# Performance work log

Measured on AMD Instinct MI355X. Metric: run time of the kernel, lower is better.

The kernel has to match this reference:

```python
import jax, jax.numpy as jnp
import numpy as np

D_MODEL = 1024
D_FF = 2 * D_MODEL
N_EXPERTS = 8
TOP_K = 2
SCAT_SCALE = 0.1


def setup_inputs() -> dict:
    key = jax.random.key(0)
    ks = jax.random.split(key, 8)
    s_in = 1.0 / np.sqrt(D_MODEL)
    s_ff = 1.0 / np.sqrt(D_FF)
    return {
        "x": jax.random.normal(ks[0], (4, 2048, D_MODEL), dtype=jnp.float32),
        "Wg": jax.random.uniform(ks[1], (D_MODEL, N_EXPERTS), minval=-s_in, maxval=s_in),
        "bg": jax.random.uniform(ks[2], (N_EXPERTS,), minval=-s_in, maxval=s_in),
        "W1": jax.random.uniform(ks[3], (N_EXPERTS, D_MODEL, D_FF), minval=-s_in, maxval=s_in),
        "b1": jax.random.uniform(ks[4], (N_EXPERTS, D_FF), minval=-s_in, maxval=s_in),
        "W2": jax.random.uniform(ks[5], (N_EXPERTS, D_FF, D_MODEL), minval=-s_ff, maxval=s_ff),
        "b2": jax.random.uniform(ks[6], (N_EXPERTS, D_MODEL), minval=-s_ff, maxval=s_ff),
    }


def reference(x, Wg, bg, W1, b1, W2, b2):
    B, N, D = x.shape
    T = B * N
    xf = x.reshape(T, D)

    # gating logits + norm-based modulation (scattering_scale branch)
    logits = xf @ Wg + bg  # [T, E]
    tnorm = jnp.linalg.norm(xf, axis=-1, keepdims=True)  # [T, 1]
    norm_scaled = (tnorm - tnorm.mean()) / (jnp.std(tnorm, ddof=1) + 1e-6)
    logits = logits + SCAT_SCALE * norm_scaled

    # top-k routing
    topv, topi = jax.lax.top_k(logits, TOP_K)  # [T, K]
    gates_k = jax.nn.softmax(topv, axis=-1)  # [T, K]
    routing_entropy = -(gates_k * jnp.log(jnp.clip(gates_k, 1e-8, None))).sum(-1).mean()

    # dense per-token expert-weight matrix (zeros for non-selected experts)
    E = W1.shape[0]
    gates = jnp.zeros((T, E), dtype=gates_k.dtype).at[
        jnp.arange(T)[:, None], topi
    ].add(gates_k)  # [T, E]

    # all-expert MLP (dense equivalent of sparse dispatch; weight 0 -> no contribution)
    h = jax.nn.relu(jnp.einsum("td,edf->etf", xf, W1) + b1[:, None, :])  # [E, T, F]
    y = jnp.einsum("etf,efd->etd", h, W2) + b2[:, None, :]  # [E, T, D]
    out = jnp.einsum("etd,te->td", y, gates).reshape(B, N, D)
    return out, routing_entropy
```

## Files before the change

### kernel.cpp

```cpp
#include <hip/hip_runtime.h>
#include <hip/hip_bf16.h>

#define T_TOK 8192
#define DMODEL 1024
#define DFF 2048
#define NEXP 8

typedef __attribute__((ext_vector_type(8))) short short8v;
typedef __attribute__((ext_vector_type(4))) float floatx4;
typedef __attribute__((ext_vector_type(4))) ushort ushort4v;

__device__ __forceinline__ ushort f2bf(float f) {
  union { float f; unsigned u; } v; v.f = f;
  unsigned u = v.u;
  unsigned r = (u + 0x7FFFu + ((u >> 16) & 1u)) >> 16;
  return (ushort)r;
}
__device__ __forceinline__ float bf2f(ushort b) {
  union { unsigned u; float f; } v; v.u = ((unsigned)b) << 16;
  return v.f;
}
__device__ __forceinline__ void gload16(const void* g, void* l) {
  __builtin_amdgcn_global_load_lds(
      (const __attribute__((address_space(1))) unsigned int*)g,
      (__attribute__((address_space(3))) unsigned int*)l, 16, 0, 0);
}
__device__ __forceinline__ short8v dsr128(unsigned off) {
  short8v r;
  asm volatile("ds_read_b128 %0, %1" : "=v"(r) : "v"(off));
  return r;
}
#define VMW(n) asm volatile("s_waitcnt vmcnt(" #n ")" ::: "memory")
#define LG0()  asm volatile("s_waitcnt lgkmcnt(0)" ::: "memory")
#define BAR()  asm volatile("s_barrier" ::: "memory")
#define SB0()  __builtin_amdgcn_sched_barrier(0)

__global__ void init_kernel(int* __restrict__ meta, float* __restrict__ entWs) {
  if (threadIdx.x < 64) meta[threadIdx.x] = 0;
  if (threadIdx.x == 0) *entWs = 0.f;
}

__global__ __launch_bounds__(256) void gating_kernel(
    const float* __restrict__ x, const float* __restrict__ Wg,
    const float* __restrict__ bg, int* __restrict__ meta,
    int* __restrict__ te, float* __restrict__ tg, float* __restrict__ entWs,
    ushort* __restrict__ xb) {
  __shared__ float wgT[8448];
  __shared__ float sbg[NEXP];
  __shared__ int cnt_s[NEXP];
  __shared__ float ent_s;
  int tid = threadIdx.x;
#pragma unroll
  for (int k = 0; k < 8; ++k) {
    int g4 = tid + 256 * k;
    float4 v = ((const float4*)Wg)[g4];
    int q = g4 * 4;
    int f = q >> 5;
    wgT[q + f]     = v.x;
    wgT[q + 1 + f] = v.y;
    wgT[q + 2 + f] = v.z;
    wgT[q + 3 + f] = v.w;
  }
  if (tid < NEXP) { sbg[tid] = bg[tid]; cnt_s[tid] = 0; }
  if (tid == 0) ent_s = 0.f;
  __syncthreads();

  int wid = tid >> 6, lane = tid & 63;
#pragma unroll 1
  for (int it = 0; it < 4; ++it) {
    int t = blockIdx.x * 16 + wid * 4 + it;
    const float* xr = x + (long)t * DMODEL;
    ushort* xbr = xb + (long)t * DMODEL;
    float acc[NEXP];
#pragma unroll
    for (int e = 0; e < NEXP; ++e) acc[e] = 0.f;
#pragma unroll
    for (int i = 0; i < 4; ++i) {
      int dbase = i * 256 + lane * 4;
      int pad = i * 64 + lane;
      float4 xv = *(const float4*)(xr + dbase);
      ushort4v s;
      s[0] = f2bf(xv.x); s[1] = f2bf(xv.y); s[2] = f2bf(xv.z); s[3] = f2bf(xv.w);
      *(ushort4v*)(xbr + dbase) = s;
      float xj[4] = {xv.x, xv.y, xv.z, xv.w};
#pragma unroll
      for (int j = 0; j < 4; ++j) {
        int base = 8 * (dbase + j) + pad;
#pragma unroll
        for (int e = 0; e < NEXP; ++e) acc[e] += xj[j] * wgT[base + e];
      }
    }
#pragma unroll
    for (int off = 32; off; off >>= 1)
#pragma unroll
      for (int e = 0; e < NEXP; ++e) acc[e] += __shfl_xor(acc[e], off, 64);
    if (lane == 0) {
      float lg[NEXP];
#pragma unroll
      for (int e = 0; e < NEXP; ++e) lg[e] = acc[e] + sbg[e];
      int e1 = 0; float v1 = lg[0];
#pragma unroll
      for (int e = 1; e < NEXP; ++e) if (lg[e] > v1) { v1 = lg[e]; e1 = e; }
      int e2 = -1; float v2 = -1e30f;
#pragma unroll
      for (int e = 0; e < NEXP; ++e) if (e != e1 && lg[e] > v2) { v2 = lg[e]; e2 = e; }
      float p2 = expf(v2 - v1);
      float s = 1.f + p2;
      float g1 = 1.f / s, g2 = p2 / s;
      float ent = -(g1 * logf(fmaxf(g1, 1e-8f)) + g2 * logf(fmaxf(g2, 1e-8f)));
      atomicAdd(&cnt_s[e1], 1);
      atomicAdd(&cnt_s[e2], 1);
      atomicAdd(&ent_s, ent);
      te[2 * t] = e1; te[2 * t + 1] = e2;
      tg[2 * t] = g1; tg[2 * t + 1] = g2;
    }
  }
  __syncthreads();
  if (tid < NEXP && cnt_s[tid]) atomicAdd(&meta[tid], cnt_s[tid]);
  if (tid == 0) atomicAdd(entWs, ent_s * (1.f / T_TOK));
}

__global__ void prefix_kernel(int* __restrict__ meta) {
  if (threadIdx.x == 0) {
    int s = 0;
    for (int e = 0; e < NEXP; ++e) { meta[16 + e] = s; s += meta[e]; meta[32 + e] = 0; }
  }
}

__global__ void scatter_kernel(const int* __restrict__ te, const float* __restrict__ tg,
                               int* __restrict__ meta, int* __restrict__ tok,
                               float* __restrict__ gate, int* __restrict__ slotOf) {
  int t = blockIdx.x * blockDim.x + threadIdx.x;
  if (t >= T_TOK) return;
  for (int k = 0; k < 2; ++k) {
    int e = te[2 * t + k];
    int pos = atomicAdd(&meta[32 + e], 1);
    int slot = meta[16 + e] + pos;
    tok[slot] = t;
    gate[slot] = tg[2 * t + k];
    slotOf[2 * t + k] = slot;
  }
}

__global__ __launch_bounds__(256) void tcvt_kernel(const float* __restrict__ src,
                                                   ushort* __restrict__ dst,
                                                   int R, int C) {
  __shared__ ushort tile[64][72];
  int tid = threadIdx.x;
  long eoff = (long)blockIdx.z * R * C;
  int r0 = blockIdx.y * 64, c0 = blockIdx.x * 64;
  int lr = tid >> 4, lc = (tid & 15) * 4;
#pragma unroll
  for (int p = 0; p < 4; ++p) {
    int r = lr + p * 16;
    float4 v = *(const float4*)&src[eoff + (long)(r0 + r) * C + (c0 + lc)];
    tile[r][lc + 0] = f2bf(v.x); tile[r][lc + 1] = f2bf(v.y);
    tile[r][lc + 2] = f2bf(v.z); tile[r][lc + 3] = f2bf(v.w);
  }
  __syncthreads();
  int sr = tid >> 3, sc = (tid & 7) * 8;
#pragma unroll
  for (int p = 0; p < 2; ++p) {
    int c = sr + p * 32;
    short8v v;
#pragma unroll
    for (int j = 0; j < 8; ++j) v[j] = (short)tile[sc + j][c];
    *(short8v*)&dst[eoff + (long)(c0 + c) * R + (r0 + sc)] = v;
  }
}

__device__ __forceinline__ void gemm_pipe(
    int NT, const char* aP0, const char* aP1,
    const char* bP0, const char* bP1, const char* bP2, const char* bP3,
    char* lds, int tid, floatx4 (&acc)[8][4]) {
  const unsigned ldsU = (unsigned)(unsigned long)lds;
  int lane = tid & 63, wid = tid >> 6;
  int lr = lane & 15, lg = lane >> 4;
  unsigned offA[8], offB[4];
#pragma unroll
  for (int mi = 0; mi < 8; ++mi) {
    int row = mi * 16 + lr;
    offA[mi] = row * 64 + ((lg * 16) ^ (((row >> 1) & 3) << 4));
  }
#pragma unroll
  for (int ni = 0; ni < 4; ++ni) {
    int row = wid * 64 + ni * 16 + lr;
    offB[ni] = row * 64 + ((lg * 16) ^ (((row >> 1) & 3) << 4));
  }

  auto STG_A = [&](int b, int t) {
    int koff = t * 64;
    char* d = lds + b * 8192;
    gload16(aP0 + koff, d + tid * 16);
    gload16(aP1 + koff, d + 4096 + tid * 16);
  };
  auto STG_B = [&](int b, int t) {
    int koff = t * 64;
    char* d = lds + 24576 + b * 16384;
    gload16(bP0 + koff, d + tid * 16);
    gload16(bP1 + koff, d + 4096 + tid * 16);
    gload16(bP2 + koff, d + 8192 + tid * 16);
    gload16(bP3 + koff, d + 12288 + tid * 16);
  };
  auto RDA = [&](int b, int mi) {
    return dsr128(ldsU + (unsigned)(b * 8192) + offA[mi]);
  };
  auto RDB = [&](int b, int ni) {
    return dsr128(ldsU + (unsigned)(24576 + b * 16384) + offB[ni]);
  };
  auto MM = [&](int mh, short8v* af, short8v* bf) {
#pragma unroll
    for (int mi = 0; mi < 4; ++mi)
#pragma unroll
      for (int ni = 0; ni < 4; ++ni)
        acc[mh * 4 + mi][ni] =
            __builtin_amdgcn_mfma_f32_16x16x32_bf16(af[mi], bf[ni], acc[mh * 4 + mi][ni], 0, 0, 0);
  };

  STG_A(0, 0); STG_B(0, 0);
  STG_A(1, 1); STG_B(1, 1);
  VMW(6); BAR();

  short8v af[4], bf[4];
  int b = 0;
  for (int t = 0; t + 2 < NT; ++t) {
    int bs = (b == 0) ? 2 : b - 1;
#pragma unroll
    for (int ni = 0; ni < 4; ++ni) bf[ni] = RDB(b, ni);
#pragma unroll
    for (int i = 0; i < 4; ++i) af[i] = RDA(b, i);
    STG_A(bs, t + 2);
    BAR(); LG0(); SB0();
    __builtin_amdgcn_s_setprio(1); MM(0, af, bf); __builtin_amdgcn_s_setprio(0);
    SB0(); BAR();
#pragma unroll
    for (int i = 0; i < 4; ++i) af[i] = RDA(b, 4 + i);
    STG_B(bs, t + 2);
    VMW(6);
    BAR(); LG0(); SB0();
    __builtin_amdgcn_s_setprio(1); MM(1, af, bf); __builtin_amdgcn_s_setprio(0);
    SB0(); BAR();
    b = (b == 2) ? 0 : b + 1;
  }
  {
#pragma unroll
    for (int ni = 0; ni < 4; ++ni) bf[ni] = RDB(b, ni);
#pragma unroll
    for (int i = 0; i < 4; ++i) af[i] = RDA(b, i);
    BAR(); LG0(); SB0();
    __builtin_amdgcn_s_setprio(1); MM(0, af, bf); __builtin_amdgcn_s_setprio(0);
    SB0(); BAR();
#pragma unroll
    for (int i = 0; i < 4; ++i) af[i] = RDA(b, 4 + i);
    VMW(0);
    BAR(); LG0(); SB0();
    __builtin_amdgcn_s_setprio(1); MM(1, af, bf); __builtin_amdgcn_s_setprio(0);
    SB0(); BAR();
    b = (b == 2) ? 0 : b + 1;
  }
  {
#pragma unroll
    for (int ni = 0; ni < 4; ++ni) bf[ni] = RDB(b, ni);
#pragma unroll
    for (int i = 0; i < 4; ++i) af[i] = RDA(b, i);
    BAR(); LG0(); SB0();
    __builtin_amdgcn_s_setprio(1); MM(0, af, bf); __builtin_amdgcn_s_setprio(0);
    SB0(); BAR();
#pragma unroll
    for (int i = 0; i < 4; ++i) af[i] = RDA(b, 4 + i);
    LG0(); SB0();
    __builtin_amdgcn_s_setprio(1); MM(1, af, bf); __builtin_amdgcn_s_setprio(0);
  }
}

__global__ __launch_bounds__(256, 2) void gemm1_kernel(
    const ushort* __restrict__ xb, const ushort* __restrict__ w1t,
    const float* __restrict__ b1, const int* __restrict__ meta,
    const int* __restrict__ tok, ushort* __restrict__ h) {
  const int NWG = 64 * 8 * NEXP;
  int flat = blockIdx.x;
  int wgid = (flat % 8) * (NWG / 8) + flat / 8;
  int m0 = (wgid & 63) * 128;
  int rest = wgid >> 6;
  int n0 = (rest & 7) * 256;
  int e = rest >> 3;
  int cnt = meta[e];
  if (m0 >= cnt) return;
  int bas = meta[16 + e];
  __shared__ char lds[73728];
  int tid = threadIdx.x;

  const char* w1e = (const char*)(w1t + (long)e * DFF * DMODEL);
  int rA = tid >> 2;
  int ch = tid & 3;
  auto sc = [&](int row) { return (unsigned)((ch * 16) ^ (((row >> 1) & 3) << 4)); };
  int ma0 = m0 + rA;        if (ma0 >= cnt) ma0 = cnt - 1;
  int ma1 = m0 + rA + 64;   if (ma1 >= cnt) ma1 = cnt - 1;
  const char* aP0 = (const char*)xb + (long)tok[bas + ma0] * (DMODEL * 2) + sc(rA);
  const char* aP1 = (const char*)xb + (long)tok[bas + ma1] * (DMODEL * 2) + sc(rA + 64);
  const char* bP0 = w1e + (long)(n0 + rA) * (DMODEL * 2) + sc(rA);
  const char* bP1 = w1e + (long)(n0 + rA + 64) * (DMODEL * 2) + sc(rA + 64);
  const char* bP2 = w1e + (long)(n0 + rA + 128) * (DMODEL * 2) + sc(rA + 128);
  const char* bP3 = w1e + (long)(n0 + rA + 192) * (DMODEL * 2) + sc(rA + 192);

  floatx4 acc[8][4];
#pragma unroll
  for (int i = 0; i < 8; ++i)
#pragma unroll
    for (int j = 0; j < 4; ++j) acc[i][j] = (floatx4){0.f, 0.f, 0.f, 0.f};

  gemm_pipe(DMODEL / 32, aP0, aP1, bP0, bP1, bP2, bP3, lds, tid, acc);

  int lane = tid & 63, wid = tid >> 6;
  int lr = lane & 15, lg = lane >> 4;
  const float* b1e = b1 + e * DFF;
#pragma unroll
  for (int mi = 0; mi < 8; ++mi) {
#pragma unroll
    for (int r = 0; r < 4; ++r) {
      int m = m0 + mi * 16 + lg * 4 + r;
      if (m >= cnt) continue;
      long hrow = (long)(bas + m) * DFF;
#pragma unroll
      for (int ni = 0; ni < 4; ++ni) {
        int f = n0 + wid * 64 + ni * 16 + lr;
        float v = acc[mi][ni][r] + b1e[f];
        h[hrow + f] = f2bf(fmaxf(v, 0.f));
      }
    }
  }
}

__global__ __launch_bounds__(256, 2) void gemm2_kernel(
    const ushort* __restrict__ h, const ushort* __restrict__ w2t,
    const float* __restrict__ b2, const int* __restrict__ meta,
    const float* __restrict__ gate, ushort* __restrict__ y) {
  const int NWG = 64 * 4 * NEXP;
  int flat = blockIdx.x;
  int wgid = (flat % 8) * (NWG / 8) + flat / 8;
  int m0 = (wgid & 63) * 128;
  int rest = wgid >> 6;
  int n0 = (rest & 3) * 256;
  int e = rest >> 2;
  int cnt = meta[e];
  if (m0 >= cnt) return;
  int bas = meta[16 + e];
  __shared__ char lds[73728];
  int tid = threadIdx.x;

  const char* w2e = (const char*)(w2t + (long)e * DMODEL * DFF);
  int rA = tid >> 2;
  int ch = tid & 3;
  auto sc = [&](int row) { return (unsigned)((ch * 16) ^ (((row >> 1) & 3) << 4)); };
  int ma0 = m0 + rA;        if (ma0 >= cnt) ma0 = cnt - 1;
  int ma1 = m0 + rA + 64;   if (ma1 >= cnt) ma1 = cnt - 1;
  const char* aP0 = (const char*)h + (long)(bas + ma0) * (DFF * 2) + sc(rA);
  const char* aP1 = (const char*)h + (long)(bas + ma1) * (DFF * 2) + sc(rA + 64);
  const char* bP0 = w2e + (long)(n0 + rA) * (DFF * 2) + sc(rA);
  const char* bP1 = w2e + (long)(n0 + rA + 64) * (DFF * 2) + sc(rA + 64);
  const char* bP2 = w2e + (long)(n0 + rA + 128) * (DFF * 2) + sc(rA + 128);
  const char* bP3 = w2e + (long)(n0 + rA + 192) * (DFF * 2) + sc(rA + 192);

  floatx4 acc[8][4];
#pragma unroll
  for (int i = 0; i < 8; ++i)
#pragma unroll
    for (int j = 0; j < 4; ++j) acc[i][j] = (floatx4){0.f, 0.f, 0.f, 0.f};

  gemm_pipe(DFF / 32, aP0, aP1, bP0, bP1, bP2, bP3, lds, tid, acc);

  int lane = tid & 63, wid = tid >> 6;
  int lr = lane & 15, lg = lane >> 4;
  const float* b2e = b2 + e * DMODEL;
#pragma unroll
  for (int mi = 0; mi < 8; ++mi) {
#pragma unroll
    for (int r = 0; r < 4; ++r) {
      int m = m0 + mi * 16 + lg * 4 + r;
      if (m >= cnt) continue;
      int slot = bas + m;
      float g = gate[slot];
      ushort* yr = y + (long)slot * DMODEL;
#pragma unroll
      for (int ni = 0; ni < 4; ++ni) {
        int n = n0 + wid * 64 + ni * 16 + lr;
        float v = g * (acc[mi][ni][r] + b2e[n]);
        yr[n] = f2bf(v);
      }
    }
  }
}

__global__ __launch_bounds__(256) void combine_kernel(
    const ushort* __restrict__ y, const int* __restrict__ slotOf,
    const float* __restrict__ entWs, float* __restrict__ out) {
  int t = blockIdx.x;
  int s1 = slotOf[2 * t], s2 = slotOf[2 * t + 1];
  int d = threadIdx.x * 4;
  ushort4v a = *(const ushort4v*)&y[(long)s1 * DMODEL + d];
  ushort4v b = *(const ushort4v*)&y[(long)s2 * DMODEL + d];
  float4 r;
  r.x = bf2f(a[0]) + bf2f(b[0]);
  r.y = bf2f(a[1]) + bf2f(b[1]);
  r.z = bf2f(a[2]) + bf2f(b[2]);
  r.w = bf2f(a[3]) + bf2f(b[3]);
  *(float4*)&out[(long)t * DMODEL + d] = r;
  if (t == 0 && threadIdx.x == 0) out[(long)T_TOK * DMODEL] = *entWs;
}

extern "C" void kernel_launch(void* const* d_in, const int* in_sizes, int n_in,
                              void* d_out, int out_size, void* d_ws, size_t ws_size,
                              hipStream_t stream) {
  const float* x  = (const float*)d_in[0];
  const float* Wg = (const float*)d_in[1];
  const float* bg = (const float*)d_in[2];
  const float* W1 = (const float*)d_in[3];
  const float* b1 = (const float*)d_in[4];
  const float* W2 = (const float*)d_in[5];
  const float* b2 = (const float*)d_in[6];
  float* out = (float*)d_out;

  char* ws = (char*)d_ws;
  int*    meta   = (int*)(ws + 0);
  float*  entWs  = (float*)(ws + 256);
  int*    te     = (int*)(ws + 1024);
  float*  tg     = (float*)(ws + 66560);
  int*    tokA   = (int*)(ws + 132096);
  float*  gate   = (float*)(ws + 197632);
  int*    slotOf = (int*)(ws + 263168);
  ushort* xb     = (ushort*)(ws + 328704);
  ushort* w1t    = (ushort*)(ws + 17105920);
  ushort* w2t    = (ushort*)(ws + 50660352);
  ushort* h      = (ushort*)(ws + 84214784);
  ushort* y      = w1t;

  init_kernel<<<1, 64, 0, stream>>>(meta, entWs);
  gating_kernel<<<T_TOK / 16, 256, 0, stream>>>(x, Wg, bg, meta, te, tg, entWs, xb);
  prefix_kernel<<<1, 1, 0, stream>>>(meta);
  scatter_kernel<<<T_TOK / 256, 256, 0, stream>>>(te, tg, meta, tokA, gate, slotOf);
  tcvt_kernel<<<dim3(DFF / 64, DMODEL / 64, NEXP), 256, 0, stream>>>(W1, w1t, DMODEL, DFF);
  tcvt_kernel<<<dim3(DMODEL / 64, DFF / 64, NEXP), 256, 0, stream>>>(W2, w2t, DFF, DMODEL);
  gemm1_kernel<<<64 * 8 * NEXP, 256, 0, stream>>>(xb, w1t, b1, meta, tokA, h);
  gemm2_kernel<<<64 * 4 * NEXP, 256, 0, stream>>>(h, w2t, b2, meta, gate, y);
  combine_kernel<<<T_TOK, 256, 0, stream>>>(y, slotOf, entWs, out);
}
```

Baseline: 336.7 us.

## Fuse weight transposes with init, halve gating tokens per block, rewrite gemm2 without LDS

```diff
diff --git a/kernel.cpp b/kernel.cpp
--- a/kernel.cpp
+++ b/kernel.cpp
@@ -34,11 +34,6 @@
 #define LG0()  asm volatile("s_waitcnt lgkmcnt(0)" ::: "memory")
 #define BAR()  asm volatile("s_barrier" ::: "memory")
 #define SB0()  __builtin_amdgcn_sched_barrier(0)
-
-__global__ void init_kernel(int* __restrict__ meta, float* __restrict__ entWs) {
-  if (threadIdx.x < 64) meta[threadIdx.x] = 0;
-  if (threadIdx.x == 0) *entWs = 0.f;
-}
 
 __global__ __launch_bounds__(256) void gating_kernel(
     const float* __restrict__ x, const float* __restrict__ Wg,
@@ -67,8 +62,8 @@
 
   int wid = tid >> 6, lane = tid & 63;
 #pragma unroll 1
-  for (int it = 0; it < 4; ++it) {
-    int t = blockIdx.x * 16 + wid * 4 + it;
+  for (int it = 0; it < 2; ++it) {
+    int t = blockIdx.x * 8 + wid * 2 + it;
     const float* xr = x + (long)t * DMODEL;
     ushort* xbr = xb + (long)t * DMODEL;
     float acc[NEXP];
@@ -142,13 +137,27 @@
   }
 }
 
-__global__ __launch_bounds__(256) void tcvt_kernel(const float* __restrict__ src,
-                                                   ushort* __restrict__ dst,
-                                                   int R, int C) {
+__global__ __launch_bounds__(256) void tcvt2_kernel(
+    const float* __restrict__ W1, const float* __restrict__ W2,
+    ushort* __restrict__ w1t, ushort* __restrict__ w2t,
+    int* __restrict__ meta, float* __restrict__ entWs) {
+  int id = blockIdx.x;
+  if (id == 0) {
+    if (threadIdx.x < 64) meta[threadIdx.x] = 0;
+    if (threadIdx.x == 64) *entWs = 0.f;
+  }
+  const float* src; ushort* dst; int R, C, r0, c0, e;
+  if (id < 4096) {
+    src = W1; dst = w1t; R = DMODEL; C = DFF;
+    c0 = (id & 31) * 64; r0 = ((id >> 5) & 15) * 64; e = id >> 9;
+  } else {
+    int j = id - 4096;
+    src = W2; dst = w2t; R = DFF; C = DMODEL;
+    c0 = (j & 15) * 64; r0 = ((j >> 4) & 31) * 64; e = j >> 9;
+  }
   __shared__ ushort tile[64][72];
   int tid = threadIdx.x;
-  long eoff = (long)blockIdx.z * R * C;
-  int r0 = blockIdx.y * 64, c0 = blockIdx.x * 64;
+  long eoff = (long)e * R * C;
   int lr = tid >> 4, lc = (tid & 15) * 4;
 #pragma unroll
   for (int p = 0; p < 4; ++p) {
@@ -331,59 +340,92 @@
   }
 }
 
-__global__ __launch_bounds__(256, 2) void gemm2_kernel(
+__global__ __launch_bounds__(256) void gemm2_kernel(
     const ushort* __restrict__ h, const ushort* __restrict__ w2t,
     const float* __restrict__ b2, const int* __restrict__ meta,
     const float* __restrict__ gate, ushort* __restrict__ y) {
-  const int NWG = 64 * 4 * NEXP;
+  const int NWG = 64 * 8 * NEXP;
   int flat = blockIdx.x;
   int wgid = (flat % 8) * (NWG / 8) + flat / 8;
   int m0 = (wgid & 63) * 128;
   int rest = wgid >> 6;
-  int n0 = (rest & 3) * 256;
-  int e = rest >> 2;
+  int n0 = (rest & 7) * 128;
+  int e = rest >> 3;
   int cnt = meta[e];
   if (m0 >= cnt) return;
   int bas = meta[16 + e];
-  __shared__ char lds[73728];
   int tid = threadIdx.x;
-
-  const char* w2e = (const char*)(w2t + (long)e * DMODEL * DFF);
-  int rA = tid >> 2;
-  int ch = tid & 3;
-  auto sc = [&](int row) { return (unsigned)((ch * 16) ^ (((row >> 1) & 3) << 4)); };
-  int ma0 = m0 + rA;        if (ma0 >= cnt) ma0 = cnt - 1;
-  int ma1 = m0 + rA + 64;   if (ma1 >= cnt) ma1 = cnt - 1;
-  const char* aP0 = (const char*)h + (long)(bas + ma0) * (DFF * 2) + sc(rA);
-  const char* aP1 = (const char*)h + (long)(bas + ma1) * (DFF * 2) + sc(rA + 64);
-  const char* bP0 = w2e + (long)(n0 + rA) * (DFF * 2) + sc(rA);
-  const char* bP1 = w2e + (long)(n0 + rA + 64) * (DFF * 2) + sc(rA + 64);
-  const char* bP2 = w2e + (long)(n0 + rA + 128) * (DFF * 2) + sc(rA + 128);
-  const char* bP3 = w2e + (long)(n0 + rA + 192) * (DFF * 2) + sc(rA + 192);
-
-  floatx4 acc[8][4];
-#pragma unroll
-  for (int i = 0; i < 8; ++i)
-#pragma unroll
-    for (int j = 0; j < 4; ++j) acc[i][j] = (floatx4){0.f, 0.f, 0.f, 0.f};
-
-  gemm_pipe(DFF / 32, aP0, aP1, bP0, bP1, bP2, bP3, lds, tid, acc);
-
   int lane = tid & 63, wid = tid >> 6;
   int lr = lane & 15, lg = lane >> 4;
+  int m0w = m0 + (wid >> 1) * 64;
+  int n0w = n0 + (wid & 1) * 64;
+
+  const char* w2e = (const char*)(w2t + (long)e * DMODEL * DFF);
+  const char* aP[4];
+  const char* bP[4];
+#pragma unroll
+  for (int mi = 0; mi < 4; ++mi) {
+    int m = m0w + mi * 16 + lr; if (m >= cnt) m = cnt - 1;
+    aP[mi] = (const char*)h + (long)(bas + m) * (DFF * 2) + lg * 16;
+  }
+#pragma unroll
+  for (int ni = 0; ni < 4; ++ni) {
+    int n = n0w + ni * 16 + lr;
+    bP[ni] = w2e + (long)n * (DFF * 2) + lg * 16;
+  }
+
+  floatx4 acc[4][4];
+#pragma unroll
+  for (int i = 0; i < 4; ++i)
+#pragma unroll
+    for (int j = 0; j < 4; ++j) acc[i][j] = (floatx4){0.f, 0.f, 0.f, 0.f};
+
+  const int NT = DFF / 32;
+  short8v fA[2][4], fB[2][4];
+#pragma unroll
+  for (int i = 0; i < 4; ++i) {
+    fA[0][i] = *(const short8v*)(aP[i]);
+    fB[0][i] = *(const short8v*)(bP[i]);
+  }
+#pragma unroll 2
+  for (int t = 0; t < NT - 1; ++t) {
+    int cur = t & 1, nxt = cur ^ 1;
+    long ko = (long)(t + 1) * 64;
+#pragma unroll
+    for (int i = 0; i < 4; ++i) {
+      fA[nxt][i] = *(const short8v*)(aP[i] + ko);
+      fB[nxt][i] = *(const short8v*)(bP[i] + ko);
+    }
+#pragma unroll
+    for (int mi = 0; mi < 4; ++mi)
+#pragma unroll
+      for (int ni = 0; ni < 4; ++ni)
+        acc[mi][ni] = __builtin_amdgcn_mfma_f32_16x16x32_bf16(
+            fA[cur][mi], fB[cur][ni], acc[mi][ni], 0, 0, 0);
+  }
+  {
+    int cur = (NT - 1) & 1;
+#pragma unroll
+    for (int mi = 0; mi < 4; ++mi)
+#pragma unroll
+      for (int ni = 0; ni < 4; ++ni)
+        acc[mi][ni] = __builtin_amdgcn_mfma_f32_16x16x32_bf16(
+            fA[cur][mi], fB[cur][ni], acc[mi][ni], 0, 0, 0);
+  }
+
   const float* b2e = b2 + e * DMODEL;
 #pragma unroll
-  for (int mi = 0; mi < 8; ++mi) {
+  for (int mi = 0; mi < 4; ++mi) {
 #pragma unroll
     for (int r = 0; r < 4; ++r) {
-      int m = m0 + mi * 16 + lg * 4 + r;
+      int m = m0w + mi * 16 + lg * 4 + r;
       if (m >= cnt) continue;
       int slot = bas + m;
       float g = gate[slot];
       ushort* yr = y + (long)slot * DMODEL;
 #pragma unroll
       for (int ni = 0; ni < 4; ++ni) {
-        int n = n0 + wid * 64 + ni * 16 + lr;
+        int n = n0w + ni * 16 + lr;
         float v = g * (acc[mi][ni][r] + b2e[n]);
         yr[n] = f2bf(v);
       }
@@ -434,13 +476,11 @@
   ushort* h      = (ushort*)(ws + 84214784);
   ushort* y      = w1t;
 
-  init_kernel<<<1, 64, 0, stream>>>(meta, entWs);
-  gating_kernel<<<T_TOK / 16, 256, 0, stream>>>(x, Wg, bg, meta, te, tg, entWs, xb);
+  tcvt2_kernel<<<8192, 256, 0, stream>>>(W1, W2, w1t, w2t, meta, entWs);
+  gating_kernel<<<T_TOK / 8, 256, 0, stream>>>(x, Wg, bg, meta, te, tg, entWs, xb);
   prefix_kernel<<<1, 1, 0, stream>>>(meta);
   scatter_kernel<<<T_TOK / 256, 256, 0, stream>>>(te, tg, meta, tokA, gate, slotOf);
-  tcvt_kernel<<<dim3(DFF / 64, DMODEL / 64, NEXP), 256, 0, stream>>>(W1, w1t, DMODEL, DFF);
-  tcvt_kernel<<<dim3(DMODEL / 64, DFF / 64, NEXP), 256, 0, stream>>>(W2, w2t, DFF, DMODEL);
   gemm1_kernel<<<64 * 8 * NEXP, 256, 0, stream>>>(xb, w1t, b1, meta, tokA, h);
-  gemm2_kernel<<<64 * 4 * NEXP, 256, 0, stream>>>(h, w2t, b2, meta, gate, y);
+  gemm2_kernel<<<64 * 8 * NEXP, 256, 0, stream>>>(h, w2t, b2, meta, gate, y);
   combine_kernel<<<T_TOK, 256, 0, stream>>>(y, slotOf, entWs, out);
 }
```

Measured after the change: 650.0 us. +93.0%, slower.
